# Performance work log

Hardware: AMD Instinct MI355X
Metric: run time of the kernel (lower is better)

## Reference

```python
import jax, jax.numpy as jnp
import numpy as np
from jax import lax

D_MODEL, D_INNER, D_STATE, DT_RANK, D_CONV = 512, 1024, 16, 32, 4
B, L = 4, 1024

def setup_inputs() -> dict:
    key = jax.random.key(0)
    ks = jax.random.split(key, 10)
    s = lambda k, shp, sc=0.02: jax.random.normal(k, shp, jnp.float32) * sc
    x = jax.random.normal(ks[0], (B, L, D_MODEL), jnp.float32)
    in_proj_w = s(ks[1], (2 * D_INNER, D_MODEL))
    conv_w = s(ks[2], (D_INNER, 1, D_CONV), 0.1)
    conv_b = jnp.zeros((D_INNER,), jnp.float32)
    x_proj_w = s(ks[3], (DT_RANK + 2 * D_STATE, D_INNER))
    dt_proj_w = s(ks[4], (D_INNER, DT_RANK), DT_RANK ** -0.5)
    dt_proj_b = s(ks[5], (D_INNER,), 0.1)
    # S4D-real init: A_log = log(1..d_state) per channel
    A_log = jnp.log(jnp.tile(jnp.arange(1, D_STATE + 1, dtype=jnp.float32), (D_INNER, 1)))
    D = jnp.ones((D_INNER,), jnp.float32)
    out_proj_w = s(ks[6], (D_MODEL, D_INNER))
    return dict(x=x, in_proj_w=in_proj_w, conv_w=conv_w, conv_b=conv_b,
                x_proj_w=x_proj_w, dt_proj_w=dt_proj_w, dt_proj_b=dt_proj_b,
                A_log=A_log, D=D, out_proj_w=out_proj_w)

def _mamba_fwd(x, in_proj_w, conv_w, conv_b, x_proj_w, dt_proj_w, dt_proj_b, A_log, D, out_proj_w):
    # in_proj and split into ssm branch / gate branch
    xz = jnp.einsum('bld,ed->ble', x, in_proj_w)          # [B,L,2*d_inner]
    xc, z = jnp.split(xz, 2, axis=-1)
    # depthwise causal conv1d along L (torch pads d_conv-1 both sides then slices [:L])
    xt = jnp.transpose(xc, (0, 2, 1))                      # [B,d_inner,L]
    xt = lax.conv_general_dilated(xt, conv_w, (1,), [(D_CONV - 1, 0)],
                                  feature_group_count=D_INNER,
                                  dimension_numbers=('NCH', 'OIH', 'NCH'))
    xc = jnp.transpose(xt + conv_b[None, :, None], (0, 2, 1))  # [B,L,d_inner]
    xc = jax.nn.silu(xc)
    # input-dependent SSM params
    dbc = jnp.einsum('bld,ed->ble', xc, x_proj_w)          # [B,L,dt_rank+2*d_state]
    dt, Bm, Cm = jnp.split(dbc, [DT_RANK, DT_RANK + D_STATE], axis=-1)
    delta = jax.nn.softplus(jnp.einsum('blr,dr->bld', dt, dt_proj_w) + dt_proj_b)  # [B,L,d_inner]
    A = -jnp.exp(A_log)                                    # [d_inner,d_state]
    deltaA = jnp.exp(delta[..., None] * A)                 # [B,L,d_inner,d_state]
    deltaBx = delta[..., None] * Bm[:, :, None, :] * xc[..., None]
    # parallel (associative) scan: h_t = deltaA_t * h_{t-1} + deltaBx_t
    def combine(c1, c2):
        a1, b1 = c1
        a2, b2 = c2
        return a2 * a1, a2 * b1 + b2
    _, h = lax.associative_scan(combine, (deltaA, deltaBx), axis=1)
    y = jnp.sum(h * Cm[:, :, None, :], axis=-1) + D * xc   # [B,L,d_inner]
    y = y * jax.nn.silu(z)
    return jnp.einsum('bld,ed->ble', y, out_proj_w)        # [B,L,d_model]

def reference(x, in_proj_w, conv_w, conv_b, x_proj_w, dt_proj_w, dt_proj_b, A_log, D, out_proj_w):
    return _mamba_fwd(x, in_proj_w, conv_w, conv_b, x_proj_w, dt_proj_w, dt_proj_b, A_log, D, out_proj_w)
```

## Files before the change

kernel.cpp:

```cpp
#include <hip/hip_runtime.h>
#include <cstddef>
#include <cstdint>

#define DMODEL 512
#define DINNER 1024
#define DSTATE 16
#define DTRANK 32
#define DCONV  4
#define NB     4
#define NL     1024
#define NR     (NB * NL)
#define CH     16
#define NCHUNK (NL / CH)
#define LOG2E  1.4426950408889634f
#define LN2    0.6931471805599453f

typedef __attribute__((ext_vector_type(8))) short bf16x8;
typedef __attribute__((ext_vector_type(4))) float f32x4;

__device__ __forceinline__ unsigned short f2bf(float f) {
    unsigned u = __builtin_bit_cast(unsigned, f);
    unsigned r = u + 0x7FFFu + ((u >> 16) & 1u);
    return (unsigned short)(r >> 16);
}
__device__ __forceinline__ float bf2f(unsigned short h) {
    return __builtin_bit_cast(float, (unsigned)h << 16);
}

__device__ __forceinline__ void gload_lds16(const unsigned short* g, unsigned short* lds) {
    __builtin_amdgcn_global_load_lds(
        (const __attribute__((address_space(1))) void*)g,
        (__attribute__((address_space(3))) void*)lds, 16, 0, 0);
}

__device__ __forceinline__ void pow_chain16(float q, float* dA) {
    dA[0] = q;
    dA[1] = q * q;
    dA[2] = dA[1] * q;
    dA[3] = dA[1] * dA[1];
    dA[4] = dA[3] * q;
    dA[5] = dA[3] * dA[1];
    dA[6] = dA[3] * dA[2];
    dA[7] = dA[3] * dA[3];
    dA[8] = dA[7] * q;
    dA[9] = dA[7] * dA[1];
    dA[10] = dA[7] * dA[2];
    dA[11] = dA[7] * dA[3];
    dA[12] = dA[7] * dA[4];
    dA[13] = dA[7] * dA[5];
    dA[14] = dA[7] * dA[6];
    dA[15] = dA[7] * dA[7];
}

__global__ __launch_bounds__(256) void cast_all_kernel(
    const float* __restrict__ x, const float* __restrict__ w_in,
    const float* __restrict__ w_out, const float* __restrict__ w_xp,
    unsigned short* __restrict__ xh, unsigned short* __restrict__ wih,
    unsigned short* __restrict__ woh, unsigned short* __restrict__ xpwh)
{
    int i = blockIdx.x * 256 + threadIdx.x;
    const float* src; unsigned short* dst;
    if (i < 524288)       { src = x;     dst = xh;   }
    else if (i < 786432)  { src = w_in;  dst = wih;  i -= 524288; }
    else if (i < 917504)  { src = w_out; dst = woh;  i -= 786432; }
    else if (i < 933888)  { src = w_xp;  dst = xpwh; i -= 917504; }
    else return;
    float4 v = ((const float4*)src)[i];
    ushort4 o;
    o.x = f2bf(v.x); o.y = f2bf(v.y); o.z = f2bf(v.z); o.w = f2bf(v.w);
    ((ushort4*)dst)[i] = o;
}

template<int BN, int OUTBF>
__global__ __launch_bounds__(256) void gemm_bf16_kernel(
    const unsigned short* __restrict__ A, const unsigned short* __restrict__ Bw,
    void* __restrict__ Cv, int M, int N, int K)
{
    constexpr int BK = 64;
    constexpr int NFRAG = BN / 32;
    constexpr int BINSTR = BN / 32;
    __shared__ unsigned short As[128 * BK];
    __shared__ unsigned short Bs[BN * BK];

    const int tid  = threadIdx.x;
    const int lane = tid & 63;
    const int w    = tid >> 6;
    const int wm   = w >> 1, wn = w & 1;
    const int brow = blockIdx.y * 128;
    const int bcol = blockIdx.x * BN;

    const int srcslot = (lane & 7) ^ (lane >> 3);
    const unsigned short* ag[4];
    unsigned short* al[4];
#pragma unroll
    for (int i = 0; i < 4; ++i) {
        const int r = w * 32 + i * 8 + (lane >> 3);
        ag[i] = A + (size_t)(brow + r) * K + srcslot * 8;
        al[i] = As + (w * 256 + i * 64) * 8;
    }
    const unsigned short* bg[BINSTR];
    unsigned short* bl[BINSTR];
#pragma unroll
    for (int i = 0; i < BINSTR; ++i) {
        const int r = w * 8 * BINSTR + i * 8 + (lane >> 3);
        bg[i] = Bw + (size_t)(bcol + r) * K + srcslot * 8;
        bl[i] = Bs + (w * 64 * BINSTR + i * 64) * 8;
    }

    const int fr = lane & 15;
    const int fq = lane >> 4;
    f32x4 acc[4][NFRAG] = {};

    for (int k0 = 0; k0 < K; k0 += BK) {
#pragma unroll
        for (int i = 0; i < 4; ++i) gload_lds16(ag[i] + k0, al[i]);
#pragma unroll
        for (int i = 0; i < BINSTR; ++i) gload_lds16(bg[i] + k0, bl[i]);
        __syncthreads();
#pragma unroll
        for (int ks = 0; ks < 2; ++ks) {
            bf16x8 af[4], bfr[NFRAG];
#pragma unroll
            for (int m = 0; m < 4; ++m) {
                const int r = wm * 64 + m * 16 + fr;
                const int s = (ks * 4 + fq) ^ (r & 7);
                af[m] = *(const bf16x8*)(As + r * BK + s * 8);
            }
#pragma unroll
            for (int n = 0; n < NFRAG; ++n) {
                const int r = wn * (BN / 2) + n * 16 + fr;
                const int s = (ks * 4 + fq) ^ (r & 7);
                bfr[n] = *(const bf16x8*)(Bs + r * BK + s * 8);
            }
#pragma unroll
            for (int m = 0; m < 4; ++m)
#pragma unroll
                for (int n = 0; n < NFRAG; ++n)
                    acc[m][n] = __builtin_amdgcn_mfma_f32_16x16x32_bf16(
                        af[m], bfr[n], acc[m][n], 0, 0, 0);
        }
        __syncthreads();
    }

    const int row0 = brow + wm * 64;
    const int col0 = bcol + wn * (BN / 2);
#pragma unroll
    for (int m = 0; m < 4; ++m)
#pragma unroll
        for (int n = 0; n < NFRAG; ++n)
#pragma unroll
            for (int j = 0; j < 4; ++j) {
                const size_t ci = (size_t)(row0 + m * 16 + fq * 4 + j) * N + col0 + n * 16 + fr;
                if (OUTBF) ((unsigned short*)Cv)[ci] = f2bf(acc[m][n][j]);
                else       ((float*)Cv)[ci] = acc[m][n][j];
            }
}

__global__ __launch_bounds__(256) void conv_silu_kernel(
    const unsigned short* __restrict__ xzh, const float* __restrict__ conv_w,
    const float* __restrict__ conv_b, unsigned short* __restrict__ xch)
{
    const int idx4 = blockIdx.x * 256 + threadIdx.x;
    const int e4 = idx4 & (DINNER / 4 - 1);
    const int r  = idx4 >> 8;
    const int l  = r & (NL - 1);
    const float4 cb = ((const float4*)conv_b)[e4];
    float4 w[4];
#pragma unroll
    for (int c = 0; c < 4; ++c) w[c] = ((const float4*)conv_w)[e4 * 4 + c];
    const ushort4 uz = {0, 0, 0, 0};
    const ushort4 u0 = (l >= 3) ? ((const ushort4*)(xzh + (size_t)(r - 3) * 2 * DINNER))[e4] : uz;
    const ushort4 u1 = (l >= 2) ? ((const ushort4*)(xzh + (size_t)(r - 2) * 2 * DINNER))[e4] : uz;
    const ushort4 u2 = (l >= 1) ? ((const ushort4*)(xzh + (size_t)(r - 1) * 2 * DINNER))[e4] : uz;
    const ushort4 u3 = ((const ushort4*)(xzh + (size_t)r * 2 * DINNER))[e4];
    float4 o;
    o.x = cb.x + w[0].x * bf2f(u0.x) + w[0].y * bf2f(u1.x) + w[0].z * bf2f(u2.x) + w[0].w * bf2f(u3.x);
    o.y = cb.y + w[1].x * bf2f(u0.y) + w[1].y * bf2f(u1.y) + w[1].z * bf2f(u2.y) + w[1].w * bf2f(u3.y);
    o.z = cb.z + w[2].x * bf2f(u0.z) + w[2].y * bf2f(u1.z) + w[2].z * bf2f(u2.z) + w[2].w * bf2f(u3.z);
    o.w = cb.w + w[3].x * bf2f(u0.w) + w[3].y * bf2f(u1.w) + w[3].z * bf2f(u2.w) + w[3].w * bf2f(u3.w);
    float4 s;
    s.x = o.x * __builtin_amdgcn_rcpf(1.f + __builtin_amdgcn_exp2f(-o.x * LOG2E));
    s.y = o.y * __builtin_amdgcn_rcpf(1.f + __builtin_amdgcn_exp2f(-o.y * LOG2E));
    s.z = o.z * __builtin_amdgcn_rcpf(1.f + __builtin_amdgcn_exp2f(-o.z * LOG2E));
    s.w = o.w * __builtin_amdgcn_rcpf(1.f + __builtin_amdgcn_exp2f(-o.w * LOG2E));
    ushort4 h4;
    h4.x = f2bf(s.x); h4.y = f2bf(s.y); h4.z = f2bf(s.z); h4.w = f2bf(s.w);
    ((ushort4*)xch)[idx4] = h4;
}

#define DRT 32
__global__ __launch_bounds__(256) void delta_kernel(
    const float* __restrict__ dbc, const float* __restrict__ dtw,
    const float* __restrict__ dtb, float* __restrict__ delta)
{
    __shared__ float dlds[DRT * DTRANK];
    const int t = threadIdx.x;
    const int e = blockIdx.x * 256 + t;
    const int r0 = blockIdx.y * DRT;
    for (int i = t; i < DRT * DTRANK; i += 256) {
        const int row = i >> 5, jj = i & 31;
        dlds[i] = dbc[(size_t)(r0 + row) * 64 + jj];
    }
    float4 wv[8];
    const float4* dtw4 = (const float4*)(dtw + (size_t)e * DTRANK);
#pragma unroll
    for (int q = 0; q < 8; ++q) wv[q] = dtw4[q];
    const float bias = dtb[e];
    __syncthreads();
#pragma unroll 4
    for (int row = 0; row < DRT; ++row) {
        const float4* dl4 = (const float4*)(dlds + row * DTRANK);
        float sum = bias;
#pragma unroll
        for (int q = 0; q < 8; ++q) {
            const float4 dv = dl4[q];
            const float4 w = wv[q];
            sum += dv.x * w.x + dv.y * w.y + dv.z * w.z + dv.w * w.w;
        }
        const float u = __builtin_amdgcn_exp2f(-fabsf(sum) * LOG2E);
        delta[(size_t)(r0 + row) * DINNER + e] =
            fmaxf(sum, 0.f) + __builtin_amdgcn_logf(1.f + u) * LN2;
    }
}

__global__ __launch_bounds__(256) void scanA_kernel(
    const float* __restrict__ delta, const unsigned short* __restrict__ xch,
    const float* __restrict__ dbc, const float* __restrict__ A_log,
    float* __restrict__ chunkP, float* __restrict__ chunkS)
{
    const int tid = threadIdx.x;
    const int e = blockIdx.x * 256 + tid;
    const int b = blockIdx.y, ck = blockIdx.z;
    const int rbase = b * NL + ck * CH;

    float Aes2[DSTATE];
    const float4* al4 = (const float4*)(A_log + (size_t)e * DSTATE);
#pragma unroll
    for (int q = 0; q < 4; ++q) {
        const float4 a = al4[q];
        Aes2[q * 4 + 0] = -__expf(a.x) * LOG2E;
        Aes2[q * 4 + 1] = -__expf(a.y) * LOG2E;
        Aes2[q * 4 + 2] = -__expf(a.z) * LOG2E;
        Aes2[q * 4 + 3] = -__expf(a.w) * LOG2E;
    }
    bool fast = true;
#pragma unroll
    for (int s = 1; s < DSTATE; ++s)
        fast = fast && (fabsf(Aes2[s] - (float)(s + 1) * Aes2[0]) <= 1e-4f * fabsf(Aes2[s]));

    float S[DSTATE];
#pragma unroll
    for (int s = 0; s < DSTATE; ++s) S[s] = 0.f;
    float cum = 0.f;
    const float* dp = delta + (size_t)rbase * DINNER + e;
    const unsigned short* xp = xch + (size_t)rbase * DINNER + e;
    if (fast) {
        const float a1 = Aes2[0];
        for (int l = 0; l < CH; ++l) {
            const float dl = dp[(size_t)l * DINNER];
            const float xv = bf2f(xp[(size_t)l * DINNER]);
            const float* bu = dbc + (size_t)(rbase + l) * 64 + DTRANK;
            cum += dl;
            const float common = dl * xv;
            float dA[DSTATE];
            pow_chain16(__builtin_amdgcn_exp2f(dl * a1), dA);
#pragma unroll
            for (int s = 0; s < DSTATE; ++s)
                S[s] = fmaf(dA[s], S[s], common * bu[s]);
        }
    } else {
        for (int l = 0; l < CH; ++l) {
            const float dl = dp[(size_t)l * DINNER];
            const float xv = bf2f(xp[(size_t)l * DINNER]);
            const float* bu = dbc + (size_t)(rbase + l) * 64 + DTRANK;
            cum += dl;
            const float common = dl * xv;
#pragma unroll
            for (int s = 0; s < DSTATE; ++s) {
                const float dA = __builtin_amdgcn_exp2f(dl * Aes2[s]);
                S[s] = fmaf(dA, S[s], common * bu[s]);
            }
        }
    }
    float P[DSTATE];
    if (fast) {
        pow_chain16(__builtin_amdgcn_exp2f(cum * Aes2[0]), P);
    } else {
#pragma unroll
        for (int s = 0; s < DSTATE; ++s) P[s] = __builtin_amdgcn_exp2f(cum * Aes2[s]);
    }
    const size_t oi = (((size_t)b * NCHUNK + ck) * DINNER + e) * DSTATE;
    float4* Pp = (float4*)(chunkP + oi);
    float4* Sp = (float4*)(chunkS + oi);
#pragma unroll
    for (int q = 0; q < 4; ++q) {
        float4 pv, sv;
        pv.x = P[q * 4 + 0]; pv.y = P[q * 4 + 1]; pv.z = P[q * 4 + 2]; pv.w = P[q * 4 + 3];
        sv.x = S[q * 4 + 0]; sv.y = S[q * 4 + 1]; sv.z = S[q * 4 + 2]; sv.w = S[q * 4 + 3];
        Pp[q] = pv; Sp[q] = sv;
    }
}

__global__ __launch_bounds__(256) void scanB_kernel(
    const float* __restrict__ chunkP, float* __restrict__ chunkS)
{
    const int idx = blockIdx.x * 256 + threadIdx.x;
    const int b = idx >> 14;
    const int rem = idx & (DINNER * DSTATE - 1);
    const size_t base = (size_t)b * NCHUNK * (DINNER * DSTATE) + rem;
    float h = 0.f;
#pragma unroll 8
    for (int c = 0; c < NCHUNK; ++c) {
        const size_t i = base + (size_t)c * (DINNER * DSTATE);
        const float P = chunkP[i];
        const float S = chunkS[i];
        chunkS[i] = h;
        h = fmaf(P, h, S);
    }
}

__global__ __launch_bounds__(256) void scanC_kernel(
    const unsigned short* __restrict__ xzh, const unsigned short* __restrict__ xch,
    const float* __restrict__ dbc, const float* __restrict__ A_log,
    const float* __restrict__ Dp, const float* __restrict__ hinit,
    const float* __restrict__ delta, unsigned short* __restrict__ yh)
{
    const int tid = threadIdx.x;
    const int e = blockIdx.x * 256 + tid;
    const int b = blockIdx.y, ck = blockIdx.z;
    const int rbase = b * NL + ck * CH;

    float Aes2[DSTATE];
    const float4* al4 = (const float4*)(A_log + (size_t)e * DSTATE);
#pragma unroll
    for (int q = 0; q < 4; ++q) {
        const float4 a = al4[q];
        Aes2[q * 4 + 0] = -__expf(a.x) * LOG2E;
        Aes2[q * 4 + 1] = -__expf(a.y) * LOG2E;
        Aes2[q * 4 + 2] = -__expf(a.z) * LOG2E;
        Aes2[q * 4 + 3] = -__expf(a.w) * LOG2E;
    }
    bool fast = true;
#pragma unroll
    for (int s = 1; s < DSTATE; ++s)
        fast = fast && (fabsf(Aes2[s] - (float)(s + 1) * Aes2[0]) <= 1e-4f * fabsf(Aes2[s]));

    float h[DSTATE];
    const size_t oi = (((size_t)b * NCHUNK + ck) * DINNER + e) * DSTATE;
    const float4* h4 = (const float4*)(hinit + oi);
#pragma unroll
    for (int q = 0; q < 4; ++q) {
        const float4 v = h4[q];
        h[q * 4 + 0] = v.x; h[q * 4 + 1] = v.y; h[q * 4 + 2] = v.z; h[q * 4 + 3] = v.w;
    }
    const float Dv = Dp[e];

    const float* dp = delta + (size_t)rbase * DINNER + e;
    const unsigned short* xp = xch + (size_t)rbase * DINNER + e;
    const unsigned short* zp = xzh + (size_t)rbase * (2 * DINNER) + DINNER + e;
    unsigned short* yp = yh + (size_t)rbase * DINNER + e;

    if (fast) {
        const float a1 = Aes2[0];
        for (int l = 0; l < CH; ++l) {
            const float dl = dp[(size_t)l * DINNER];
            const float xv = bf2f(xp[(size_t)l * DINNER]);
            const float zv = bf2f(zp[(size_t)l * 2 * DINNER]);
            const float* bu = dbc + (size_t)(rbase + l) * 64 + DTRANK;
            const float common = dl * xv;
            float dA[DSTATE];
            pow_chain16(__builtin_amdgcn_exp2f(dl * a1), dA);
            float y = 0.f;
#pragma unroll
            for (int s = 0; s < DSTATE; ++s) {
                h[s] = fmaf(dA[s], h[s], common * bu[s]);
                y = fmaf(h[s], bu[DSTATE + s], y);
            }
            y = fmaf(Dv, xv, y);
            const float sig = __builtin_amdgcn_rcpf(1.f + __builtin_amdgcn_exp2f(-zv * LOG2E));
            yp[(size_t)l * DINNER] = f2bf(y * (zv * sig));
        }
    } else {
        for (int l = 0; l < CH; ++l) {
            const float dl = dp[(size_t)l * DINNER];
            const float xv = bf2f(xp[(size_t)l * DINNER]);
            const float zv = bf2f(zp[(size_t)l * 2 * DINNER]);
            const float* bu = dbc + (size_t)(rbase + l) * 64 + DTRANK;
            const float common = dl * xv;
            float y = 0.f;
#pragma unroll
            for (int s = 0; s < DSTATE; ++s) {
                const float dA = __builtin_amdgcn_exp2f(dl * Aes2[s]);
                h[s] = fmaf(dA, h[s], common * bu[s]);
                y = fmaf(h[s], bu[DSTATE + s], y);
            }
            y = fmaf(Dv, xv, y);
            const float sig = __builtin_amdgcn_rcpf(1.f + __builtin_amdgcn_exp2f(-zv * LOG2E));
            yp[(size_t)l * DINNER] = f2bf(y * (zv * sig));
        }
    }
}

extern "C" void kernel_launch(void* const* d_in, const int* in_sizes, int n_in,
                              void* d_out, int out_size, void* d_ws, size_t ws_size,
                              hipStream_t stream)
{
    const float* x          = (const float*)d_in[0];
    const float* in_proj_w  = (const float*)d_in[1];
    const float* conv_w     = (const float*)d_in[2];
    const float* conv_b     = (const float*)d_in[3];
    const float* x_proj_w   = (const float*)d_in[4];
    const float* dt_proj_w  = (const float*)d_in[5];
    const float* dt_proj_b  = (const float*)d_in[6];
    const float* A_log      = (const float*)d_in[7];
    const float* Dp         = (const float*)d_in[8];
    const float* out_proj_w = (const float*)d_in[9];
    float* out = (float*)d_out;

    float* ws     = (float*)d_ws;
    float* dbc    = ws;
    float* yb     = dbc + (size_t)NR * 64;
    float* chunkS = yb + (size_t)NR * DINNER;
    float* chunkP = chunkS + (size_t)NB * NCHUNK * DINNER * DSTATE;
    unsigned short* xzh  = (unsigned short*)(chunkP + (size_t)NB * NCHUNK * DINNER * DSTATE);
    unsigned short* xch  = xzh + (size_t)NR * 2 * DINNER;
    unsigned short* yh   = xch + (size_t)NR * DINNER;
    unsigned short* xh   = yh + (size_t)NR * DINNER;
    unsigned short* wih  = xh + (size_t)NR * DMODEL;
    unsigned short* woh  = wih + (size_t)2 * DINNER * DMODEL;
    unsigned short* xpwh = woh + (size_t)DMODEL * DINNER;

    cast_all_kernel<<<(933888 + 255) / 256, 256, 0, stream>>>(
        x, in_proj_w, out_proj_w, x_proj_w, xh, wih, woh, xpwh);

    gemm_bf16_kernel<128, 1><<<dim3(2 * DINNER / 128, NR / 128), 256, 0, stream>>>(
        xh, wih, xzh, NR, 2 * DINNER, DMODEL);
    conv_silu_kernel<<<NR * DINNER / 1024, 256, 0, stream>>>(xzh, conv_w, conv_b, xch);
    gemm_bf16_kernel<64, 0><<<dim3(1, NR / 128), 256, 0, stream>>>(
        xch, xpwh, dbc, NR, 64, DINNER);
    delta_kernel<<<dim3(DINNER / 256, NR / DRT), 256, 0, stream>>>(
        dbc, dt_proj_w, dt_proj_b, yb);
    scanA_kernel<<<dim3(DINNER / 256, NB, NCHUNK), 256, 0, stream>>>(
        yb, xch, dbc, A_log, chunkP, chunkS);
    scanB_kernel<<<NB * DINNER * DSTATE / 256, 256, 0, stream>>>(chunkP, chunkS);
    scanC_kernel<<<dim3(DINNER / 256, NB, NCHUNK), 256, 0, stream>>>(
        xzh, xch, dbc, A_log, Dp, chunkS, yb, yh);
    gemm_bf16_kernel<64, 0><<<dim3(DMODEL / 64, NR / 128), 256, 0, stream>>>(
        yh, woh, out, NR, DMODEL, DINNER);
}
```

Baseline: 134.8 us.

## Fuse conv+SiLU into x_proj GEMM with split-K, recompute conv in scans, widen in_proj tile

Removes the separate conv_silu kernel and the xch intermediate buffer. The x_proj GEMM now computes the causal conv and SiLU on the fly into LDS, splits K four ways and accumulates into a zeroed dbc with atomics. The scan kernels recompute the conv and SiLU from xzh instead of reading xch. The in_proj GEMM uses a 512-thread 128x256 tile, and the scan chunk length doubles from 16 to 32. In exchange there is extra recompute, atomic traffic, a memset, and fewer scan blocks.

```diff
diff --git a/kernel.cpp b/kernel.cpp
--- a/kernel.cpp
+++ b/kernel.cpp
@@ -6,11 +6,10 @@
 #define DINNER 1024
 #define DSTATE 16
 #define DTRANK 32
-#define DCONV  4
 #define NB     4
 #define NL     1024
 #define NR     (NB * NL)
-#define CH     16
+#define CH     32
 #define NCHUNK (NL / CH)
 #define LOG2E  1.4426950408889634f
 #define LN2    0.6931471805599453f
@@ -34,22 +33,11 @@
 }
 
 __device__ __forceinline__ void pow_chain16(float q, float* dA) {
-    dA[0] = q;
-    dA[1] = q * q;
-    dA[2] = dA[1] * q;
-    dA[3] = dA[1] * dA[1];
-    dA[4] = dA[3] * q;
-    dA[5] = dA[3] * dA[1];
-    dA[6] = dA[3] * dA[2];
-    dA[7] = dA[3] * dA[3];
-    dA[8] = dA[7] * q;
-    dA[9] = dA[7] * dA[1];
-    dA[10] = dA[7] * dA[2];
-    dA[11] = dA[7] * dA[3];
-    dA[12] = dA[7] * dA[4];
-    dA[13] = dA[7] * dA[5];
-    dA[14] = dA[7] * dA[6];
-    dA[15] = dA[7] * dA[7];
+    dA[0] = q;  dA[1] = q * q;  dA[2] = dA[1] * q;  dA[3] = dA[1] * dA[1];
+    dA[4] = dA[3] * q;  dA[5] = dA[3] * dA[1];  dA[6] = dA[3] * dA[2];
+    dA[7] = dA[3] * dA[3];  dA[8] = dA[7] * q;  dA[9] = dA[7] * dA[1];
+    dA[10] = dA[7] * dA[2];  dA[11] = dA[7] * dA[3];  dA[12] = dA[7] * dA[4];
+    dA[13] = dA[7] * dA[5];  dA[14] = dA[7] * dA[6];  dA[15] = dA[7] * dA[7];
 }
 
 __global__ __launch_bounds__(256) void cast_all_kernel(
@@ -71,23 +59,100 @@
     ((ushort4*)dst)[i] = o;
 }
 
-template<int BN, int OUTBF>
-__global__ __launch_bounds__(256) void gemm_bf16_kernel(
+__global__ __launch_bounds__(512) void gemm1_wide_kernel(
     const unsigned short* __restrict__ A, const unsigned short* __restrict__ Bw,
-    void* __restrict__ Cv, int M, int N, int K)
+    unsigned short* __restrict__ C, int M, int N, int K)
 {
     constexpr int BK = 64;
-    constexpr int NFRAG = BN / 32;
-    constexpr int BINSTR = BN / 32;
     __shared__ unsigned short As[128 * BK];
-    __shared__ unsigned short Bs[BN * BK];
+    __shared__ unsigned short Bs[256 * BK];
+
+    const int tid  = threadIdx.x;
+    const int lane = tid & 63;
+    const int w    = tid >> 6;
+    const int wm   = w >> 2, wn = w & 3;
+    const int brow = blockIdx.y * 128;
+    const int bcol = blockIdx.x * 256;
+
+    const int srcslot = (lane & 7) ^ (lane >> 3);
+    const unsigned short* ag[2];
+    unsigned short* al[2];
+#pragma unroll
+    for (int i = 0; i < 2; ++i) {
+        const int r = w * 16 + i * 8 + (lane >> 3);
+        ag[i] = A + (size_t)(brow + r) * K + srcslot * 8;
+        al[i] = As + (w * 16 + i * 8) * BK;
+    }
+    const unsigned short* bg[4];
+    unsigned short* bl[4];
+#pragma unroll
+    for (int i = 0; i < 4; ++i) {
+        const int r = w * 32 + i * 8 + (lane >> 3);
+        bg[i] = Bw + (size_t)(bcol + r) * K + srcslot * 8;
+        bl[i] = Bs + (w * 32 + i * 8) * BK;
+    }
+
+    const int fr = lane & 15;
+    const int fq = lane >> 4;
+    f32x4 acc[4][4] = {};
+
+    for (int k0 = 0; k0 < K; k0 += BK) {
+#pragma unroll
+        for (int i = 0; i < 2; ++i) gload_lds16(ag[i] + k0, al[i]);
+#pragma unroll
+        for (int i = 0; i < 4; ++i) gload_lds16(bg[i] + k0, bl[i]);
+        __syncthreads();
+#pragma unroll
+        for (int ks = 0; ks < 2; ++ks) {
+            bf16x8 af[4], bfr[4];
+#pragma unroll
+            for (int m = 0; m < 4; ++m) {
+                const int r = wm * 64 + m * 16 + fr;
+                const int s = (ks * 4 + fq) ^ (r & 7);
+                af[m] = *(const bf16x8*)(As + r * BK + s * 8);
+            }
+#pragma unroll
+            for (int n = 0; n < 4; ++n) {
+                const int r = wn * 64 + n * 16 + fr;
+                const int s = (ks * 4 + fq) ^ (r & 7);
+                bfr[n] = *(const bf16x8*)(Bs + r * BK + s * 8);
+            }
+#pragma unroll
+            for (int m = 0; m < 4; ++m)
+#pragma unroll
+                for (int n = 0; n < 4; ++n)
+                    acc[m][n] = __builtin_amdgcn_mfma_f32_16x16x32_bf16(
+                        af[m], bfr[n], acc[m][n], 0, 0, 0);
+        }
+        __syncthreads();
+    }
+
+    const int row0 = brow + wm * 64;
+    const int col0 = bcol + wn * 64;
+#pragma unroll
+    for (int m = 0; m < 4; ++m)
+#pragma unroll
+        for (int n = 0; n < 4; ++n)
+#pragma unroll
+            for (int j = 0; j < 4; ++j)
+                C[(size_t)(row0 + m * 16 + fq * 4 + j) * N + col0 + n * 16 + fr] =
+                    f2bf(acc[m][n][j]);
+}
+
+__global__ __launch_bounds__(256) void gemm2_kernel(
+    const unsigned short* __restrict__ A, const unsigned short* __restrict__ Bw,
+    float* __restrict__ C, int M, int N, int K)
+{
+    constexpr int BK = 64;
+    __shared__ unsigned short As[128 * BK];
+    __shared__ unsigned short Bs[64 * BK];
 
     const int tid  = threadIdx.x;
     const int lane = tid & 63;
     const int w    = tid >> 6;
     const int wm   = w >> 1, wn = w & 1;
     const int brow = blockIdx.y * 128;
-    const int bcol = blockIdx.x * BN;
+    const int bcol = blockIdx.x * 64;
 
     const int srcslot = (lane & 7) ^ (lane >> 3);
     const unsigned short* ag[4];
@@ -96,30 +161,30 @@
     for (int i = 0; i < 4; ++i) {
         const int r = w * 32 + i * 8 + (lane >> 3);
         ag[i] = A + (size_t)(brow + r) * K + srcslot * 8;
-        al[i] = As + (w * 256 + i * 64) * 8;
-    }
-    const unsigned short* bg[BINSTR];
-    unsigned short* bl[BINSTR];
-#pragma unroll
-    for (int i = 0; i < BINSTR; ++i) {
-        const int r = w * 8 * BINSTR + i * 8 + (lane >> 3);
-        bg[i] = Bw + (size_t)(bcol + r) * K + srcslot * 8;
-        bl[i] = Bs + (w * 64 * BINSTR + i * 64) * 8;
+        al[i] = As + (w * 32 + i * 8) * BK;
+    }
+    const int rB = w * 16 + (lane >> 3);
+    const unsigned short* bg[2];
+    unsigned short* bl[2];
+#pragma unroll
+    for (int i = 0; i < 2; ++i) {
+        bg[i] = Bw + (size_t)(bcol + rB + i * 8) * K + srcslot * 8;
+        bl[i] = Bs + (w * 16 + i * 8) * BK;
     }
 
     const int fr = lane & 15;
     const int fq = lane >> 4;
-    f32x4 acc[4][NFRAG] = {};
+    f32x4 acc[4][2] = {};
 
     for (int k0 = 0; k0 < K; k0 += BK) {
 #pragma unroll
         for (int i = 0; i < 4; ++i) gload_lds16(ag[i] + k0, al[i]);
 #pragma unroll
-        for (int i = 0; i < BINSTR; ++i) gload_lds16(bg[i] + k0, bl[i]);
+        for (int i = 0; i < 2; ++i) gload_lds16(bg[i] + k0, bl[i]);
         __syncthreads();
 #pragma unroll
         for (int ks = 0; ks < 2; ++ks) {
-            bf16x8 af[4], bfr[NFRAG];
+            bf16x8 af[4], bfr[2];
 #pragma unroll
             for (int m = 0; m < 4; ++m) {
                 const int r = wm * 64 + m * 16 + fr;
@@ -127,15 +192,15 @@
                 af[m] = *(const bf16x8*)(As + r * BK + s * 8);
             }
 #pragma unroll
-            for (int n = 0; n < NFRAG; ++n) {
-                const int r = wn * (BN / 2) + n * 16 + fr;
+            for (int n = 0; n < 2; ++n) {
+                const int r = wn * 32 + n * 16 + fr;
                 const int s = (ks * 4 + fq) ^ (r & 7);
                 bfr[n] = *(const bf16x8*)(Bs + r * BK + s * 8);
             }
 #pragma unroll
             for (int m = 0; m < 4; ++m)
 #pragma unroll
-                for (int n = 0; n < NFRAG; ++n)
+                for (int n = 0; n < 2; ++n)
                     acc[m][n] = __builtin_amdgcn_mfma_f32_16x16x32_bf16(
                         af[m], bfr[n], acc[m][n], 0, 0, 0);
         }
@@ -143,49 +208,140 @@
     }
 
     const int row0 = brow + wm * 64;
-    const int col0 = bcol + wn * (BN / 2);
+    const int col0 = bcol + wn * 32;
 #pragma unroll
     for (int m = 0; m < 4; ++m)
 #pragma unroll
-        for (int n = 0; n < NFRAG; ++n)
-#pragma unroll
-            for (int j = 0; j < 4; ++j) {
-                const size_t ci = (size_t)(row0 + m * 16 + fq * 4 + j) * N + col0 + n * 16 + fr;
-                if (OUTBF) ((unsigned short*)Cv)[ci] = f2bf(acc[m][n][j]);
-                else       ((float*)Cv)[ci] = acc[m][n][j];
-            }
-}
-
-__global__ __launch_bounds__(256) void conv_silu_kernel(
+        for (int n = 0; n < 2; ++n)
+#pragma unroll
+            for (int j = 0; j < 4; ++j)
+                C[(size_t)(row0 + m * 16 + fq * 4 + j) * N + col0 + n * 16 + fr] = acc[m][n][j];
+}
+
+#define KS 4
+__global__ __launch_bounds__(256) void xprojconv_kernel(
     const unsigned short* __restrict__ xzh, const float* __restrict__ conv_w,
-    const float* __restrict__ conv_b, unsigned short* __restrict__ xch)
-{
-    const int idx4 = blockIdx.x * 256 + threadIdx.x;
-    const int e4 = idx4 & (DINNER / 4 - 1);
-    const int r  = idx4 >> 8;
-    const int l  = r & (NL - 1);
-    const float4 cb = ((const float4*)conv_b)[e4];
-    float4 w[4];
-#pragma unroll
-    for (int c = 0; c < 4; ++c) w[c] = ((const float4*)conv_w)[e4 * 4 + c];
-    const ushort4 uz = {0, 0, 0, 0};
-    const ushort4 u0 = (l >= 3) ? ((const ushort4*)(xzh + (size_t)(r - 3) * 2 * DINNER))[e4] : uz;
-    const ushort4 u1 = (l >= 2) ? ((const ushort4*)(xzh + (size_t)(r - 2) * 2 * DINNER))[e4] : uz;
-    const ushort4 u2 = (l >= 1) ? ((const ushort4*)(xzh + (size_t)(r - 1) * 2 * DINNER))[e4] : uz;
-    const ushort4 u3 = ((const ushort4*)(xzh + (size_t)r * 2 * DINNER))[e4];
-    float4 o;
-    o.x = cb.x + w[0].x * bf2f(u0.x) + w[0].y * bf2f(u1.x) + w[0].z * bf2f(u2.x) + w[0].w * bf2f(u3.x);
-    o.y = cb.y + w[1].x * bf2f(u0.y) + w[1].y * bf2f(u1.y) + w[1].z * bf2f(u2.y) + w[1].w * bf2f(u3.y);
-    o.z = cb.z + w[2].x * bf2f(u0.z) + w[2].y * bf2f(u1.z) + w[2].z * bf2f(u2.z) + w[2].w * bf2f(u3.z);
-    o.w = cb.w + w[3].x * bf2f(u0.w) + w[3].y * bf2f(u1.w) + w[3].z * bf2f(u2.w) + w[3].w * bf2f(u3.w);
-    float4 s;
-    s.x = o.x * __builtin_amdgcn_rcpf(1.f + __builtin_amdgcn_exp2f(-o.x * LOG2E));
-    s.y = o.y * __builtin_amdgcn_rcpf(1.f + __builtin_amdgcn_exp2f(-o.y * LOG2E));
-    s.z = o.z * __builtin_amdgcn_rcpf(1.f + __builtin_amdgcn_exp2f(-o.z * LOG2E));
-    s.w = o.w * __builtin_amdgcn_rcpf(1.f + __builtin_amdgcn_exp2f(-o.w * LOG2E));
-    ushort4 h4;
-    h4.x = f2bf(s.x); h4.y = f2bf(s.y); h4.z = f2bf(s.z); h4.w = f2bf(s.w);
-    ((ushort4*)xch)[idx4] = h4;
+    const float* __restrict__ conv_b, const unsigned short* __restrict__ xpwh,
+    float* __restrict__ dbc)
+{
+    constexpr int BK = 64;
+    __shared__ unsigned short As[128 * BK];
+    __shared__ unsigned short Bs[64 * BK];
+
+    const int tid  = threadIdx.x;
+    const int lane = tid & 63;
+    const int w    = tid >> 6;
+    const int wm   = w >> 1, wn = w & 1;
+    const int brow = blockIdx.x * 128;
+    const int kbase = blockIdx.y * (DINNER / KS);
+
+    const int srcslot = (lane & 7) ^ (lane >> 3);
+    const unsigned short* bg[2];
+    unsigned short* bl[2];
+#pragma unroll
+    for (int i = 0; i < 2; ++i) {
+        const int r = w * 16 + i * 8 + (lane >> 3);
+        bg[i] = xpwh + (size_t)r * DINNER + kbase + srcslot * 8;
+        bl[i] = Bs + (w * 16 + i * 8) * BK;
+    }
+
+    const int cg = tid & 7;
+    const int rg = tid >> 3;
+    const int base = brow + rg * 4;
+    const int lb = base & (NL - 1);
+
+    const int fr = lane & 15;
+    const int fq = lane >> 4;
+    f32x4 acc[4][2] = {};
+
+    for (int it = 0; it < DINNER / KS / BK; ++it) {
+        const int k0 = kbase + it * BK;
+        {
+            const int ecol = k0 + cg * 8;
+            float cw[4][8], acc4[4][8];
+#pragma unroll
+            for (int c = 0; c < 8; ++c) {
+                const float4 w4 = *(const float4*)(conv_w + (size_t)(ecol + c) * 4);
+                cw[0][c] = w4.x; cw[1][c] = w4.y; cw[2][c] = w4.z; cw[3][c] = w4.w;
+                const float bb = conv_b[ecol + c];
+                acc4[0][c] = bb; acc4[1][c] = bb; acc4[2][c] = bb; acc4[3][c] = bb;
+            }
+#pragma unroll
+            for (int j = 0; j < 7; ++j) {
+                float in8[8];
+                if (lb + j - 3 >= 0) {
+                    const bf16x8 raw = *(const bf16x8*)(
+                        xzh + (size_t)(base + j - 3) * 2 * DINNER + ecol);
+#pragma unroll
+                    for (int c = 0; c < 8; ++c) in8[c] = bf2f((unsigned short)raw[c]);
+                } else {
+#pragma unroll
+                    for (int c = 0; c < 8; ++c) in8[c] = 0.f;
+                }
+                const int dr0 = (j - 3 > 0) ? (j - 3) : 0;
+                const int dr1 = (j < 3) ? j : 3;
+#pragma unroll
+                for (int dr = 0; dr < 4; ++dr) {
+                    if (dr < dr0 || dr > dr1) continue;
+                    const int k = j - dr;
+#pragma unroll
+                    for (int c = 0; c < 8; ++c)
+                        acc4[dr][c] = fmaf(cw[k][c], in8[c], acc4[dr][c]);
+                }
+            }
+#pragma unroll
+            for (int dr = 0; dr < 4; ++dr) {
+                const int rr = rg * 4 + dr;
+                bf16x8 pk;
+#pragma unroll
+                for (int c = 0; c < 8; ++c) {
+                    const float v = acc4[dr][c];
+                    const float s = v * __builtin_amdgcn_rcpf(
+                        1.f + __builtin_amdgcn_exp2f(-v * LOG2E));
+                    pk[c] = (short)f2bf(s);
+                }
+                *(bf16x8*)(As + rr * BK + ((cg ^ (rr & 7)) * 8)) = pk;
+            }
+        }
+#pragma unroll
+        for (int i = 0; i < 2; ++i) gload_lds16(bg[i] + it * BK, bl[i]);
+        __syncthreads();
+#pragma unroll
+        for (int ks = 0; ks < 2; ++ks) {
+            bf16x8 af[4], bfr[2];
+#pragma unroll
+            for (int m = 0; m < 4; ++m) {
+                const int r = wm * 64 + m * 16 + fr;
+                const int s = (ks * 4 + fq) ^ (r & 7);
+                af[m] = *(const bf16x8*)(As + r * BK + s * 8);
+            }
+#pragma unroll
+            for (int n = 0; n < 2; ++n) {
+                const int r = wn * 32 + n * 16 + fr;
+                const int s = (ks * 4 + fq) ^ (r & 7);
+                bfr[n] = *(const bf16x8*)(Bs + r * BK + s * 8);
+            }
+#pragma unroll
+            for (int m = 0; m < 4; ++m)
+#pragma unroll
+                for (int n = 0; n < 2; ++n)
+                    acc[m][n] = __builtin_amdgcn_mfma_f32_16x16x32_bf16(
+                        af[m], bfr[n], acc[m][n], 0, 0, 0);
+        }
+        __syncthreads();
+    }
+
+    const int row0 = brow + wm * 64;
+    const int col0 = wn * 32;
+#pragma unroll
+    for (int m = 0; m < 4; ++m)
+#pragma unroll
+        for (int n = 0; n < 2; ++n)
+#pragma unroll
+            for (int j = 0; j < 4; ++j)
+                unsafeAtomicAdd(
+                    &dbc[(size_t)(row0 + m * 16 + fq * 4 + j) * 64 + col0 + n * 16 + fr],
+                    acc[m][n][j]);
 }
 
 #define DRT 32
@@ -224,7 +380,8 @@
 }
 
 __global__ __launch_bounds__(256) void scanA_kernel(
-    const float* __restrict__ delta, const unsigned short* __restrict__ xch,
+    const float* __restrict__ delta, const unsigned short* __restrict__ xzh,
+    const float* __restrict__ conv_w, const float* __restrict__ conv_b,
     const float* __restrict__ dbc, const float* __restrict__ A_log,
     float* __restrict__ chunkP, float* __restrict__ chunkS)
 {
@@ -232,6 +389,14 @@
     const int e = blockIdx.x * 256 + tid;
     const int b = blockIdx.y, ck = blockIdx.z;
     const int rbase = b * NL + ck * CH;
+    const int lbase = ck * CH;
+
+    const float4 cwv = *(const float4*)(conv_w + (size_t)e * 4);
+    const float cbv = conv_b[e];
+    const unsigned short* xzp = xzh + (size_t)rbase * 2 * DINNER + e;
+    float xm1 = (lbase >= 1) ? bf2f(*(xzp - 2 * DINNER)) : 0.f;
+    float xm2 = (lbase >= 2) ? bf2f(*(xzp - 4 * DINNER)) : 0.f;
+    float xm3 = (lbase >= 3) ? bf2f(*(xzp - 6 * DINNER)) : 0.f;
 
     float Aes2[DSTATE];
     const float4* al4 = (const float4*)(A_log + (size_t)e * DSTATE);
@@ -253,38 +418,30 @@
     for (int s = 0; s < DSTATE; ++s) S[s] = 0.f;
     float cum = 0.f;
     const float* dp = delta + (size_t)rbase * DINNER + e;
-    const unsigned short* xp = xch + (size_t)rbase * DINNER + e;
-    if (fast) {
-        const float a1 = Aes2[0];
-        for (int l = 0; l < CH; ++l) {
-            const float dl = dp[(size_t)l * DINNER];
-            const float xv = bf2f(xp[(size_t)l * DINNER]);
-            const float* bu = dbc + (size_t)(rbase + l) * 64 + DTRANK;
-            cum += dl;
-            const float common = dl * xv;
-            float dA[DSTATE];
+    const float a1 = Aes2[0];
+    for (int l = 0; l < CH; ++l) {
+        const float cur = bf2f(xzp[(size_t)l * 2 * DINNER]);
+        const float cv = cbv + cwv.x * xm3 + cwv.y * xm2 + cwv.z * xm1 + cwv.w * cur;
+        const float xv = cv * __builtin_amdgcn_rcpf(1.f + __builtin_amdgcn_exp2f(-cv * LOG2E));
+        xm3 = xm2; xm2 = xm1; xm1 = cur;
+        const float dl = dp[(size_t)l * DINNER];
+        const float* bu = dbc + (size_t)(rbase + l) * 64 + DTRANK;
+        cum += dl;
+        const float common = dl * xv;
+        float dA[DSTATE];
+        if (fast) {
             pow_chain16(__builtin_amdgcn_exp2f(dl * a1), dA);
-#pragma unroll
-            for (int s = 0; s < DSTATE; ++s)
-                S[s] = fmaf(dA[s], S[s], common * bu[s]);
-        }
-    } else {
-        for (int l = 0; l < CH; ++l) {
-            const float dl = dp[(size_t)l * DINNER];
-            const float xv = bf2f(xp[(size_t)l * DINNER]);
-            const float* bu = dbc + (size_t)(rbase + l) * 64 + DTRANK;
-            cum += dl;
-            const float common = dl * xv;
-#pragma unroll
-            for (int s = 0; s < DSTATE; ++s) {
-                const float dA = __builtin_amdgcn_exp2f(dl * Aes2[s]);
-                S[s] = fmaf(dA, S[s], common * bu[s]);
-            }
-        }
+        } else {
+#pragma unroll
+            for (int s = 0; s < DSTATE; ++s) dA[s] = __builtin_amdgcn_exp2f(dl * Aes2[s]);
+        }
+#pragma unroll
+        for (int s = 0; s < DSTATE; ++s)
+            S[s] = fmaf(dA[s], S[s], common * bu[s]);
     }
     float P[DSTATE];
     if (fast) {
-        pow_chain16(__builtin_amdgcn_exp2f(cum * Aes2[0]), P);
+        pow_chain16(__builtin_amdgcn_exp2f(cum * a1), P);
     } else {
 #pragma unroll
         for (int s = 0; s < DSTATE; ++s) P[s] = __builtin_amdgcn_exp2f(cum * Aes2[s]);
@@ -320,15 +477,24 @@
 }
 
 __global__ __launch_bounds__(256) void scanC_kernel(
-    const unsigned short* __restrict__ xzh, const unsigned short* __restrict__ xch,
+    const float* __restrict__ delta, const unsigned short* __restrict__ xzh,
+    const float* __restrict__ conv_w, const float* __restrict__ conv_b,
     const float* __restrict__ dbc, const float* __restrict__ A_log,
     const float* __restrict__ Dp, const float* __restrict__ hinit,
-    const float* __restrict__ delta, unsigned short* __restrict__ yh)
+    unsigned short* __restrict__ yh)
 {
     const int tid = threadIdx.x;
     const int e = blockIdx.x * 256 + tid;
     const int b = blockIdx.y, ck = blockIdx.z;
     const int rbase = b * NL + ck * CH;
+    const int lbase = ck * CH;
+
+    const float4 cwv = *(const float4*)(conv_w + (size_t)e * 4);
+    const float cbv = conv_b[e];
+    const unsigned short* xzp = xzh + (size_t)rbase * 2 * DINNER + e;
+    float xm1 = (lbase >= 1) ? bf2f(*(xzp - 2 * DINNER)) : 0.f;
+    float xm2 = (lbase >= 2) ? bf2f(*(xzp - 4 * DINNER)) : 0.f;
+    float xm3 = (lbase >= 3) ? bf2f(*(xzp - 6 * DINNER)) : 0.f;
 
     float Aes2[DSTATE];
     const float4* al4 = (const float4*)(A_log + (size_t)e * DSTATE);
@@ -354,50 +520,35 @@
         h[q * 4 + 0] = v.x; h[q * 4 + 1] = v.y; h[q * 4 + 2] = v.z; h[q * 4 + 3] = v.w;
     }
     const float Dv = Dp[e];
-
     const float* dp = delta + (size_t)rbase * DINNER + e;
-    const unsigned short* xp = xch + (size_t)rbase * DINNER + e;
-    const unsigned short* zp = xzh + (size_t)rbase * (2 * DINNER) + DINNER + e;
     unsigned short* yp = yh + (size_t)rbase * DINNER + e;
-
-    if (fast) {
-        const float a1 = Aes2[0];
-        for (int l = 0; l < CH; ++l) {
-            const float dl = dp[(size_t)l * DINNER];
-            const float xv = bf2f(xp[(size_t)l * DINNER]);
-            const float zv = bf2f(zp[(size_t)l * 2 * DINNER]);
-            const float* bu = dbc + (size_t)(rbase + l) * 64 + DTRANK;
-            const float common = dl * xv;
-            float dA[DSTATE];
+    const float a1 = Aes2[0];
+
+    for (int l = 0; l < CH; ++l) {
+        const float cur = bf2f(xzp[(size_t)l * 2 * DINNER]);
+        const float zv  = bf2f(xzp[(size_t)l * 2 * DINNER + DINNER]);
+        const float cv = cbv + cwv.x * xm3 + cwv.y * xm2 + cwv.z * xm1 + cwv.w * cur;
+        const float xv = cv * __builtin_amdgcn_rcpf(1.f + __builtin_amdgcn_exp2f(-cv * LOG2E));
+        xm3 = xm2; xm2 = xm1; xm1 = cur;
+        const float dl = dp[(size_t)l * DINNER];
+        const float* bu = dbc + (size_t)(rbase + l) * 64 + DTRANK;
+        const float common = dl * xv;
+        float dA[DSTATE];
+        if (fast) {
             pow_chain16(__builtin_amdgcn_exp2f(dl * a1), dA);
-            float y = 0.f;
-#pragma unroll
-            for (int s = 0; s < DSTATE; ++s) {
-                h[s] = fmaf(dA[s], h[s], common * bu[s]);
-                y = fmaf(h[s], bu[DSTATE + s], y);
-            }
-            y = fmaf(Dv, xv, y);
-            const float sig = __builtin_amdgcn_rcpf(1.f + __builtin_amdgcn_exp2f(-zv * LOG2E));
-            yp[(size_t)l * DINNER] = f2bf(y * (zv * sig));
-        }
-    } else {
-        for (int l = 0; l < CH; ++l) {
-            const float dl = dp[(size_t)l * DINNER];
-            const float xv = bf2f(xp[(size_t)l * DINNER]);
-            const float zv = bf2f(zp[(size_t)l * 2 * DINNER]);
-            const float* bu = dbc + (size_t)(rbase + l) * 64 + DTRANK;
-            const float common = dl * xv;
-            float y = 0.f;
-#pragma unroll
-            for (int s = 0; s < DSTATE; ++s) {
-                const float dA = __builtin_amdgcn_exp2f(dl * Aes2[s]);
-                h[s] = fmaf(dA, h[s], common * bu[s]);
-                y = fmaf(h[s], bu[DSTATE + s], y);
-            }
-            y = fmaf(Dv, xv, y);
-            const float sig = __builtin_amdgcn_rcpf(1.f + __builtin_amdgcn_exp2f(-zv * LOG2E));
-            yp[(size_t)l * DINNER] = f2bf(y * (zv * sig));
-        }
+        } else {
+#pragma unroll
+            for (int s = 0; s < DSTATE; ++s) dA[s] = __builtin_amdgcn_exp2f(dl * Aes2[s]);
+        }
+        float y = 0.f;
+#pragma unroll
+        for (int s = 0; s < DSTATE; ++s) {
+            h[s] = fmaf(dA[s], h[s], common * bu[s]);
+            y = fmaf(h[s], bu[DSTATE + s], y);
+        }
+        y = fmaf(Dv, xv, y);
+        const float sig = __builtin_amdgcn_rcpf(1.f + __builtin_amdgcn_exp2f(-zv * LOG2E));
+        yp[(size_t)l * DINNER] = f2bf(y * (zv * sig));
     }
 }
 
@@ -423,28 +574,28 @@
     float* chunkS = yb + (size_t)NR * DINNER;
     float* chunkP = chunkS + (size_t)NB * NCHUNK * DINNER * DSTATE;
     unsigned short* xzh  = (unsigned short*)(chunkP + (size_t)NB * NCHUNK * DINNER * DSTATE);
-    unsigned short* xch  = xzh + (size_t)NR * 2 * DINNER;
-    unsigned short* yh   = xch + (size_t)NR * DINNER;
+    unsigned short* yh   = xzh + (size_t)NR * 2 * DINNER;
     unsigned short* xh   = yh + (size_t)NR * DINNER;
     unsigned short* wih  = xh + (size_t)NR * DMODEL;
     unsigned short* woh  = wih + (size_t)2 * DINNER * DMODEL;
     unsigned short* xpwh = woh + (size_t)DMODEL * DINNER;
 
+    hipMemsetAsync(dbc, 0, (size_t)NR * 64 * sizeof(float), stream);
+
     cast_all_kernel<<<(933888 + 255) / 256, 256, 0, stream>>>(
         x, in_proj_w, out_proj_w, x_proj_w, xh, wih, woh, xpwh);
 
-    gemm_bf16_kernel<128, 1><<<dim3(2 * DINNER / 128, NR / 128), 256, 0, stream>>>(
+    gemm1_wide_kernel<<<dim3(2 * DINNER / 256, NR / 128), 512, 0, stream>>>(
         xh, wih, xzh, NR, 2 * DINNER, DMODEL);
-    conv_silu_kernel<<<NR * DINNER / 1024, 256, 0, stream>>>(xzh, conv_w, conv_b, xch);
-    gemm_bf16_kernel<64, 0><<<dim3(1, NR / 128), 256, 0, stream>>>(
-        xch, xpwh, dbc, NR, 64, DINNER);
+    xprojconv_kernel<<<dim3(NR / 128, KS), 256, 0, stream>>>(
+        xzh, conv_w, conv_b, xpwh, dbc);
     delta_kernel<<<dim3(DINNER / 256, NR / DRT), 256, 0, stream>>>(
         dbc, dt_proj_w, dt_proj_b, yb);
     scanA_kernel<<<dim3(DINNER / 256, NB, NCHUNK), 256, 0, stream>>>(
-        yb, xch, dbc, A_log, chunkP, chunkS);
+        yb, xzh, conv_w, conv_b, dbc, A_log, chunkP, chunkS);
     scanB_kernel<<<NB * DINNER * DSTATE / 256, 256, 0, stream>>>(chunkP, chunkS);
     scanC_kernel<<<dim3(DINNER / 256, NB, NCHUNK), 256, 0, stream>>>(
-        xzh, xch, dbc, A_log, Dp, chunkS, yb, yh);
-    gemm_bf16_kernel<64, 0><<<dim3(DMODEL / 64, NR / 128), 256, 0, stream>>>(
+        yb, xzh, conv_w, conv_b, dbc, A_log, Dp, chunkS, yh);
+    gemm2_kernel<<<dim3(DMODEL / 64, NR / 128), 256, 0, stream>>>(
         yh, woh, out, NR, DMODEL, DINNER);
 }
```

Result: slower. 147.4 us (+9.3%).
